# Kernel tuning notes

Measured on AMD Instinct MI355X. Metric: run time of the kernel, lower is better.

## Reference

```python
import jax, jax.numpy as jnp
import numpy as np

N_NODES = 100_000
N_EDGES = 1_600_000
HIDDEN = 64
EPS = 1e-5  # eqx.nn.RMSNorm default eps


def setup_inputs() -> dict:
    key = jax.random.key(0)
    k1, k2, k3 = jax.random.split(key, 3)
    x = jax.random.normal(k1, (N_NODES, HIDDEN), dtype=jnp.float32)
    # edges[0] = target node i, edges[1] = source node j  (a[i, j] = 1 => edge j -> i)
    edges = jax.random.randint(k2, (2, N_EDGES), 0, N_NODES, dtype=jnp.int32)
    W = jax.random.normal(k3, (HIDDEN, HIDDEN), dtype=jnp.float32) * (1.0 / np.sqrt(HIDDEN))
    b = jnp.zeros((HIDDEN,), dtype=jnp.float32)
    norm_weight = jnp.ones((HIDDEN,), dtype=jnp.float32)
    norm_bias = jnp.zeros((HIDDEN,), dtype=jnp.float32)
    return {"x": x, "edges": edges, "W": W, "b": b,
            "norm_weight": norm_weight, "norm_bias": norm_bias}


def reference(x, edges, W, b, norm_weight, norm_bias):
    n_nodes = x.shape[0]
    # vmap(Linear) + relu:  m = relu(x @ W.T + b)
    m = jax.nn.relu(jnp.einsum('nd,kd->nk', x, W) + b)
    # a @ m : sum-aggregate messages from source j into target i
    dst, src = edges[0], edges[1]
    agg = jax.ops.segment_sum(m[src], dst, num_segments=n_nodes)
    # residual + RMSNorm (per-node)
    h = x + agg
    inv_rms = jax.lax.rsqrt(jnp.mean(h * h, axis=-1, keepdims=True) + EPS)
    return norm_weight * (h * inv_rms) + norm_bias
```

## Files before the change

### kernel.cpp

```cpp
#include <hip/hip_runtime.h>
#include <hip/hip_bf16.h>

#define N_NODES 100000
#define N_EDGES 1600000
#define HID 64

#define NG 196
#define GROUPS 511
#define GSTRIDE 512
#define NREP 2
#define RCAP 2048
#define EPT 8
#define BIN_BLOCKS 391
#define LCAP 48

using bf16 = __hip_bfloat16;
typedef __attribute__((ext_vector_type(8))) short short8;
typedef __attribute__((ext_vector_type(4))) float float4v;

__device__ __forceinline__ float bfbits2f(unsigned short u) {
    union { unsigned int i; float f; } v;
    v.i = ((unsigned int)u) << 16;
    return v.f;
}
__device__ __forceinline__ unsigned short f2bfbits(float f) {
    union { float f; unsigned int i; } v;
    v.f = f;
    unsigned int r = v.i + 0x7fffu + ((v.i >> 16) & 1u);
    return (unsigned short)(r >> 16);
}

__device__ __forceinline__ void load_frag_split(const float* __restrict__ p,
                                                short8& hi, short8& lo) {
    #pragma unroll
    for (int j = 0; j < 8; ++j) {
        const float f = p[j];
        const unsigned short h = f2bfbits(f);
        hi[j] = (short)h;
        lo[j] = (short)f2bfbits(f - bfbits2f(h));
    }
}

__global__ __launch_bounds__(256) void k_linear_mfma(
    const float* __restrict__ x, const float* __restrict__ W,
    const float* __restrict__ b, bf16* __restrict__ m)
{
    const int t = threadIdx.x;
    const int wv = t >> 6, l = t & 63;
    const int c = l & 15, q = l >> 4;
    const int tile = blockIdx.x * 4 + wv;
    if (tile >= N_NODES / 16) return;
    const int nb = tile * 16;

    short8 Bhi[4][2], Blo[4][2];
    #pragma unroll
    for (int nt = 0; nt < 4; ++nt)
        #pragma unroll
        for (int ks = 0; ks < 2; ++ks)
            load_frag_split(W + (size_t)(nt * 16 + c) * HID + ks * 32 + q * 8,
                            Bhi[nt][ks], Blo[nt][ks]);

    short8 Ahi[2], Alo[2];
    #pragma unroll
    for (int ks = 0; ks < 2; ++ks)
        load_frag_split(x + (size_t)(nb + c) * HID + ks * 32 + q * 8, Ahi[ks], Alo[ks]);

    float4v acc[4];
    #pragma unroll
    for (int nt = 0; nt < 4; ++nt) {
        const float bias = b[nt * 16 + c];
        acc[nt] = (float4v){bias, bias, bias, bias};
        #pragma unroll
        for (int ks = 0; ks < 2; ++ks) {
            acc[nt] = __builtin_amdgcn_mfma_f32_16x16x32_bf16(Ahi[ks], Bhi[nt][ks], acc[nt], 0, 0, 0);
            acc[nt] = __builtin_amdgcn_mfma_f32_16x16x32_bf16(Ahi[ks], Blo[nt][ks], acc[nt], 0, 0, 0);
            acc[nt] = __builtin_amdgcn_mfma_f32_16x16x32_bf16(Alo[ks], Bhi[nt][ks], acc[nt], 0, 0, 0);
        }
    }

    unsigned short* mp = reinterpret_cast<unsigned short*>(m);
    #pragma unroll
    for (int nt = 0; nt < 4; ++nt)
        #pragma unroll
        for (int rg = 0; rg < 4; ++rg) {
            const float v = fmaxf(acc[nt][rg], 0.0f);
            mp[(size_t)(nb + q * 4 + rg) * HID + nt * 16 + c] = f2bfbits(v);
        }
}

__global__ __launch_bounds__(512) void k_bin3(
    const int* __restrict__ edges, int* __restrict__ gcur, int* __restrict__ binned)
{
    __shared__ int cnt[GSTRIDE];
    __shared__ int base[GSTRIDE];
    const int t = threadIdx.x;
    for (int i = t; i < GSTRIDE; i += 512) cnt[i] = 0;
    __syncthreads();

    const int e0 = blockIdx.x * (512 * EPT);
    int gk[EPT], pk[EPT], sl[EPT];
    #pragma unroll
    for (int k = 0; k < EPT; ++k) {
        const int e = e0 + k * 512 + t;
        if (e < N_EDGES) {
            const int dst = edges[e];
            const int src = edges[N_EDGES + e];
            const int g = (int)((unsigned)dst / NG);
            gk[k] = g;
            pk[k] = ((dst - g * NG) << 17) | src;
            sl[k] = atomicAdd(&cnt[g], 1);
        } else gk[k] = -1;
    }
    __syncthreads();
    const int r = blockIdx.x & (NREP - 1);
    for (int i = t; i < GROUPS; i += 512) {
        const int cc = cnt[i];
        base[i] = cc ? atomicAdd(&gcur[r * GSTRIDE + i], cc) : 0;
    }
    __syncthreads();
    #pragma unroll
    for (int k = 0; k < EPT; ++k) {
        if (gk[k] >= 0) {
            const int pos = base[gk[k]] + sl[k];
            if (pos < RCAP)
                binned[(size_t)(r * GSTRIDE + gk[k]) * RCAP + pos] = pk[k];
        }
    }
}

__global__ __launch_bounds__(1024, 8) void k_gather_norm5(
    const float* __restrict__ x, const bf16* __restrict__ m,
    const int* __restrict__ gcur, const int* __restrict__ binned,
    const float* __restrict__ nw, const float* __restrict__ nb,
    float* __restrict__ out)
{
    __shared__ int lcount[NG];
    __shared__ int lsrc[NG * LCAP];
    const int t = threadIdx.x;
    const int g = blockIdx.x;
    for (int i = t; i < NG; i += 1024) lcount[i] = 0;
    __syncthreads();

    #pragma unroll
    for (int rr = 0; rr < NREP; ++rr) {
        int c = gcur[rr * GSTRIDE + g];
        if (c > RCAP) c = RCAP;
        const int* reg = binned + (size_t)(rr * GSTRIDE + g) * RCAP;
        for (int i = t; i < c; i += 1024) {
            const int pr = reg[i];
            const int dl = pr >> 17;
            const int slot = atomicAdd(&lcount[dl], 1);
            if (slot < LCAP) lsrc[dl * LCAP + slot] = pr & 0x1FFFF;
        }
    }
    __syncthreads();

    const int wv = t >> 6, l = t & 63;
    const int c = l & 15;
    const int r = l >> 4;
    const ushort4* mu4 = reinterpret_cast<const ushort4*>(m);
    const float4 nw4 = reinterpret_cast<const float4*>(nw)[c];
    const float4 nb4 = reinterpret_cast<const float4*>(nb)[c];

    for (int dl = wv; dl < NG; dl += 16) {
        const int n = g * NG + dl;
        if (n >= N_NODES) break;
        int deg = lcount[dl]; if (deg > LCAP) deg = LCAP;
        const int* row = &lsrc[dl * LCAP];

        float4 a = make_float4(0.f, 0.f, 0.f, 0.f);
        int i = 0;
        for (; i + 16 <= deg; i += 16) {
            const int s0 = row[i + r];
            const int s1 = row[i + 4 + r];
            const int s2 = row[i + 8 + r];
            const int s3 = row[i + 12 + r];
            const ushort4 v0 = mu4[(size_t)s0 * 16 + c];
            const ushort4 v1 = mu4[(size_t)s1 * 16 + c];
            const ushort4 v2 = mu4[(size_t)s2 * 16 + c];
            const ushort4 v3 = mu4[(size_t)s3 * 16 + c];
            a.x += (bfbits2f(v0.x) + bfbits2f(v1.x)) + (bfbits2f(v2.x) + bfbits2f(v3.x));
            a.y += (bfbits2f(v0.y) + bfbits2f(v1.y)) + (bfbits2f(v2.y) + bfbits2f(v3.y));
            a.z += (bfbits2f(v0.z) + bfbits2f(v1.z)) + (bfbits2f(v2.z) + bfbits2f(v3.z));
            a.w += (bfbits2f(v0.w) + bfbits2f(v1.w)) + (bfbits2f(v2.w) + bfbits2f(v3.w));
        }
        for (; i < deg; i += 4) {
            const int e = i + r;
            if (e < deg) {
                const ushort4 v = mu4[(size_t)row[e] * 16 + c];
                a.x += bfbits2f(v.x);
                a.y += bfbits2f(v.y);
                a.z += bfbits2f(v.z);
                a.w += bfbits2f(v.w);
            }
        }
        a.x += __shfl_xor(a.x, 16, 64); a.x += __shfl_xor(a.x, 32, 64);
        a.y += __shfl_xor(a.y, 16, 64); a.y += __shfl_xor(a.y, 32, 64);
        a.z += __shfl_xor(a.z, 16, 64); a.z += __shfl_xor(a.z, 32, 64);
        a.w += __shfl_xor(a.w, 16, 64); a.w += __shfl_xor(a.w, 32, 64);

        const float4 x4 = reinterpret_cast<const float4*>(x)[(size_t)n * 16 + c];
        float4 h;
        h.x = x4.x + a.x; h.y = x4.y + a.y; h.z = x4.z + a.z; h.w = x4.w + a.w;
        float ss = h.x * h.x + h.y * h.y + h.z * h.z + h.w * h.w;
        ss += __shfl_xor(ss, 1, 64);
        ss += __shfl_xor(ss, 2, 64);
        ss += __shfl_xor(ss, 4, 64);
        ss += __shfl_xor(ss, 8, 64);
        const float inv = rsqrtf(ss * (1.0f / HID) + 1e-5f);
        if (r == 0) {
            float4 o;
            o.x = nw4.x * h.x * inv + nb4.x;
            o.y = nw4.y * h.y * inv + nb4.y;
            o.z = nw4.z * h.z * inv + nb4.z;
            o.w = nw4.w * h.w * inv + nb4.w;
            reinterpret_cast<float4*>(out)[(size_t)n * 16 + c] = o;
        }
    }
}

extern "C" void kernel_launch(void* const* d_in, const int* in_sizes, int n_in,
                              void* d_out, int out_size, void* d_ws, size_t ws_size,
                              hipStream_t stream) {
    const float* x     = (const float*)d_in[0];
    const int*   edges = (const int*)d_in[1];
    const float* W     = (const float*)d_in[2];
    const float* b     = (const float*)d_in[3];
    const float* nw    = (const float*)d_in[4];
    const float* nb    = (const float*)d_in[5];
    float* out = (float*)d_out;

    int*  gcur   = (int*)d_ws;
    int*  binned = (int*)((char*)d_ws + (1 << 16));
    bf16* m      = (bf16*)((char*)d_ws + (1 << 16) +
                           (size_t)NREP * GSTRIDE * RCAP * sizeof(int));

    hipMemsetAsync(gcur, 0, NREP * GSTRIDE * sizeof(int), stream);

    k_linear_mfma<<<(N_NODES / 16 + 3) / 4, 256, 0, stream>>>(x, W, b, m);
    k_bin3<<<BIN_BLOCKS, 512, 0, stream>>>(edges, gcur, binned);
    k_gather_norm5<<<GROUPS, 1024, 0, stream>>>(x, m, gcur, binned, nw, nb, out);
}
```

Before: 156.3 us.

## Fuse linear and edge binning into one launch, presplit W, batch gather loads

Replaces the memset with a small init kernel that zeroes counters and pre-splits W into bf16 hi/lo once. The linear and edge-binning kernels are merged into one heterogeneous launch of 256-thread blocks with EPT doubled, letting the two independent phases run concurrently. The linear pass drops the x low-part MFMA term, trading some accuracy for fewer MFMAs. The gather loop now issues eight clamped loads before accumulating, increasing memory-level parallelism.

```diff
diff --git a/kernel.cpp b/kernel.cpp
--- a/kernel.cpp
+++ b/kernel.cpp
@@ -10,8 +10,9 @@
 #define GSTRIDE 512
 #define NREP 2
 #define RCAP 2048
-#define EPT 8
+#define EPT 16
 #define BIN_BLOCKS 391
+#define LIN_BLOCKS 1563
 #define LCAP 48
 
 using bf16 = __hip_bfloat16;
@@ -30,105 +31,116 @@
     return (unsigned short)(r >> 16);
 }
 
-__device__ __forceinline__ void load_frag_split(const float* __restrict__ p,
-                                                short8& hi, short8& lo) {
-    #pragma unroll
-    for (int j = 0; j < 8; ++j) {
-        const float f = p[j];
+__global__ __launch_bounds__(256) void k_init(
+    const float* __restrict__ W, int* __restrict__ gcur,
+    unsigned short* __restrict__ Whi, unsigned short* __restrict__ Wlo)
+{
+    const int t = blockIdx.x * 256 + threadIdx.x;
+    for (int i = t; i < NREP * GSTRIDE; i += 512) gcur[i] = 0;
+    for (int i = t; i < HID * HID; i += 512) {
+        const float f = W[i];
         const unsigned short h = f2bfbits(f);
-        hi[j] = (short)h;
-        lo[j] = (short)f2bfbits(f - bfbits2f(h));
-    }
-}
-
-__global__ __launch_bounds__(256) void k_linear_mfma(
-    const float* __restrict__ x, const float* __restrict__ W,
-    const float* __restrict__ b, bf16* __restrict__ m)
+        Whi[i] = h;
+        Wlo[i] = f2bfbits(f - bfbits2f(h));
+    }
+}
+
+__global__ __launch_bounds__(256, 4) void k_prep2(
+    const float* __restrict__ x, const unsigned short* __restrict__ Whi,
+    const unsigned short* __restrict__ Wlo, const float* __restrict__ b,
+    bf16* __restrict__ m,
+    const int* __restrict__ edges, int* __restrict__ gcur,
+    int* __restrict__ binned)
 {
     const int t = threadIdx.x;
-    const int wv = t >> 6, l = t & 63;
-    const int c = l & 15, q = l >> 4;
-    const int tile = blockIdx.x * 4 + wv;
-    if (tile >= N_NODES / 16) return;
-    const int nb = tile * 16;
-
-    short8 Bhi[4][2], Blo[4][2];
-    #pragma unroll
-    for (int nt = 0; nt < 4; ++nt)
+
+    if (blockIdx.x < LIN_BLOCKS) {
+        const int wv = t >> 6, l = t & 63;
+        const int c = l & 15, q = l >> 4;
+        const int tile = blockIdx.x * 4 + wv;
+        if (tile >= N_NODES / 16) return;
+        const int nb = tile * 16;
+
+        const short8* whi8 = reinterpret_cast<const short8*>(Whi);
+        const short8* wlo8 = reinterpret_cast<const short8*>(Wlo);
+        short8 Bhi[4][2], Blo[4][2];
+        #pragma unroll
+        for (int nt = 0; nt < 4; ++nt)
+            #pragma unroll
+            for (int ks = 0; ks < 2; ++ks) {
+                const int fi = (nt * 16 + c) * 8 + ks * 4 + q;
+                Bhi[nt][ks] = whi8[fi];
+                Blo[nt][ks] = wlo8[fi];
+            }
+
+        const float* xrow = x + (size_t)(nb + c) * HID;
+        short8 Ahi[2];
         #pragma unroll
         for (int ks = 0; ks < 2; ++ks)
-            load_frag_split(W + (size_t)(nt * 16 + c) * HID + ks * 32 + q * 8,
-                            Bhi[nt][ks], Blo[nt][ks]);
-
-    short8 Ahi[2], Alo[2];
-    #pragma unroll
-    for (int ks = 0; ks < 2; ++ks)
-        load_frag_split(x + (size_t)(nb + c) * HID + ks * 32 + q * 8, Ahi[ks], Alo[ks]);
-
-    float4v acc[4];
-    #pragma unroll
-    for (int nt = 0; nt < 4; ++nt) {
-        const float bias = b[nt * 16 + c];
-        acc[nt] = (float4v){bias, bias, bias, bias};
-        #pragma unroll
-        for (int ks = 0; ks < 2; ++ks) {
-            acc[nt] = __builtin_amdgcn_mfma_f32_16x16x32_bf16(Ahi[ks], Bhi[nt][ks], acc[nt], 0, 0, 0);
-            acc[nt] = __builtin_amdgcn_mfma_f32_16x16x32_bf16(Ahi[ks], Blo[nt][ks], acc[nt], 0, 0, 0);
-            acc[nt] = __builtin_amdgcn_mfma_f32_16x16x32_bf16(Alo[ks], Bhi[nt][ks], acc[nt], 0, 0, 0);
-        }
-    }
-
-    unsigned short* mp = reinterpret_cast<unsigned short*>(m);
-    #pragma unroll
-    for (int nt = 0; nt < 4; ++nt)
-        #pragma unroll
-        for (int rg = 0; rg < 4; ++rg) {
-            const float v = fmaxf(acc[nt][rg], 0.0f);
-            mp[(size_t)(nb + q * 4 + rg) * HID + nt * 16 + c] = f2bfbits(v);
-        }
-}
-
-__global__ __launch_bounds__(512) void k_bin3(
-    const int* __restrict__ edges, int* __restrict__ gcur, int* __restrict__ binned)
-{
-    __shared__ int cnt[GSTRIDE];
-    __shared__ int base[GSTRIDE];
-    const int t = threadIdx.x;
-    for (int i = t; i < GSTRIDE; i += 512) cnt[i] = 0;
-    __syncthreads();
-
-    const int e0 = blockIdx.x * (512 * EPT);
-    int gk[EPT], pk[EPT], sl[EPT];
-    #pragma unroll
-    for (int k = 0; k < EPT; ++k) {
-        const int e = e0 + k * 512 + t;
-        if (e < N_EDGES) {
-            const int dst = edges[e];
-            const int src = edges[N_EDGES + e];
-            const int g = (int)((unsigned)dst / NG);
-            gk[k] = g;
-            pk[k] = ((dst - g * NG) << 17) | src;
-            sl[k] = atomicAdd(&cnt[g], 1);
-        } else gk[k] = -1;
-    }
-    __syncthreads();
-    const int r = blockIdx.x & (NREP - 1);
-    for (int i = t; i < GROUPS; i += 512) {
-        const int cc = cnt[i];
-        base[i] = cc ? atomicAdd(&gcur[r * GSTRIDE + i], cc) : 0;
-    }
-    __syncthreads();
-    #pragma unroll
-    for (int k = 0; k < EPT; ++k) {
-        if (gk[k] >= 0) {
-            const int pos = base[gk[k]] + sl[k];
-            if (pos < RCAP)
-                binned[(size_t)(r * GSTRIDE + gk[k]) * RCAP + pos] = pk[k];
-        }
-    }
-}
-
-__global__ __launch_bounds__(1024, 8) void k_gather_norm5(
+            #pragma unroll
+            for (int j = 0; j < 8; ++j)
+                Ahi[ks][j] = (short)f2bfbits(xrow[ks * 32 + q * 8 + j]);
+
+        float4v acc[4];
+        #pragma unroll
+        for (int nt = 0; nt < 4; ++nt) {
+            const float bias = b[nt * 16 + c];
+            acc[nt] = (float4v){bias, bias, bias, bias};
+            #pragma unroll
+            for (int ks = 0; ks < 2; ++ks) {
+                acc[nt] = __builtin_amdgcn_mfma_f32_16x16x32_bf16(Ahi[ks], Bhi[nt][ks], acc[nt], 0, 0, 0);
+                acc[nt] = __builtin_amdgcn_mfma_f32_16x16x32_bf16(Ahi[ks], Blo[nt][ks], acc[nt], 0, 0, 0);
+            }
+        }
+
+        unsigned short* mp = reinterpret_cast<unsigned short*>(m);
+        #pragma unroll
+        for (int nt = 0; nt < 4; ++nt)
+            #pragma unroll
+            for (int rg = 0; rg < 4; ++rg) {
+                const float v = fmaxf(acc[nt][rg], 0.0f);
+                mp[(size_t)(nb + q * 4 + rg) * HID + nt * 16 + c] = f2bfbits(v);
+            }
+    } else {
+        __shared__ int cnt[GSTRIDE];
+        __shared__ int base[GSTRIDE];
+        const int bb = blockIdx.x - LIN_BLOCKS;
+        for (int i = t; i < GSTRIDE; i += 256) cnt[i] = 0;
+        __syncthreads();
+
+        const int e0 = bb * (256 * EPT);
+        int gk[EPT], pk[EPT], sl[EPT];
+        #pragma unroll
+        for (int k = 0; k < EPT; ++k) {
+            const int e = e0 + k * 256 + t;
+            if (e < N_EDGES) {
+                const int dst = edges[e];
+                const int src = edges[N_EDGES + e];
+                const int g = (int)((unsigned)dst / NG);
+                gk[k] = g;
+                pk[k] = ((dst - g * NG) << 17) | src;
+                sl[k] = atomicAdd(&cnt[g], 1);
+            } else gk[k] = -1;
+        }
+        __syncthreads();
+        const int r = bb & (NREP - 1);
+        for (int i = t; i < GROUPS; i += 256) {
+            const int cc = cnt[i];
+            base[i] = cc ? atomicAdd(&gcur[r * GSTRIDE + i], cc) : 0;
+        }
+        __syncthreads();
+        #pragma unroll
+        for (int k = 0; k < EPT; ++k) {
+            if (gk[k] >= 0) {
+                const int pos = base[gk[k]] + sl[k];
+                if ((unsigned)pos < RCAP)
+                    binned[(size_t)(r * GSTRIDE + gk[k]) * RCAP + pos] = pk[k];
+            }
+        }
+    }
+}
+
+__global__ __launch_bounds__(1024, 8) void k_gather_norm6(
     const float* __restrict__ x, const bf16* __restrict__ m,
     const int* __restrict__ gcur, const int* __restrict__ binned,
     const float* __restrict__ nw, const float* __restrict__ nb,
@@ -169,29 +181,23 @@
         const int* row = &lsrc[dl * LCAP];
 
         float4 a = make_float4(0.f, 0.f, 0.f, 0.f);
-        int i = 0;
-        for (; i + 16 <= deg; i += 16) {
-            const int s0 = row[i + r];
-            const int s1 = row[i + 4 + r];
-            const int s2 = row[i + 8 + r];
-            const int s3 = row[i + 12 + r];
-            const ushort4 v0 = mu4[(size_t)s0 * 16 + c];
-            const ushort4 v1 = mu4[(size_t)s1 * 16 + c];
-            const ushort4 v2 = mu4[(size_t)s2 * 16 + c];
-            const ushort4 v3 = mu4[(size_t)s3 * 16 + c];
-            a.x += (bfbits2f(v0.x) + bfbits2f(v1.x)) + (bfbits2f(v2.x) + bfbits2f(v3.x));
-            a.y += (bfbits2f(v0.y) + bfbits2f(v1.y)) + (bfbits2f(v2.y) + bfbits2f(v3.y));
-            a.z += (bfbits2f(v0.z) + bfbits2f(v1.z)) + (bfbits2f(v2.z) + bfbits2f(v3.z));
-            a.w += (bfbits2f(v0.w) + bfbits2f(v1.w)) + (bfbits2f(v2.w) + bfbits2f(v3.w));
-        }
-        for (; i < deg; i += 4) {
-            const int e = i + r;
-            if (e < deg) {
-                const ushort4 v = mu4[(size_t)row[e] * 16 + c];
-                a.x += bfbits2f(v.x);
-                a.y += bfbits2f(v.y);
-                a.z += bfbits2f(v.z);
-                a.w += bfbits2f(v.w);
+        for (int i0 = 0; i0 < deg; i0 += 32) {
+            ushort4 vb[8];
+            #pragma unroll
+            for (int j = 0; j < 8; ++j) {
+                const int e = i0 + j * 4 + r;
+                const int ec = (e < deg) ? e : (deg - 1);
+                vb[j] = mu4[(size_t)row[ec] * 16 + c];
+            }
+            #pragma unroll
+            for (int j = 0; j < 8; ++j) {
+                const int e = i0 + j * 4 + r;
+                if (e < deg) {
+                    a.x += bfbits2f(vb[j].x);
+                    a.y += bfbits2f(vb[j].y);
+                    a.z += bfbits2f(vb[j].z);
+                    a.w += bfbits2f(vb[j].w);
+                }
             }
         }
         a.x += __shfl_xor(a.x, 16, 64); a.x += __shfl_xor(a.x, 32, 64);
@@ -230,14 +236,14 @@
     const float* nb    = (const float*)d_in[5];
     float* out = (float*)d_out;
 
-    int*  gcur   = (int*)d_ws;
+    int* gcur = (int*)d_ws;
+    unsigned short* Whi = (unsigned short*)((char*)d_ws + (1 << 14));
+    unsigned short* Wlo = Whi + HID * HID;
     int*  binned = (int*)((char*)d_ws + (1 << 16));
     bf16* m      = (bf16*)((char*)d_ws + (1 << 16) +
                            (size_t)NREP * GSTRIDE * RCAP * sizeof(int));
 
-    hipMemsetAsync(gcur, 0, NREP * GSTRIDE * sizeof(int), stream);
-
-    k_linear_mfma<<<(N_NODES / 16 + 3) / 4, 256, 0, stream>>>(x, W, b, m);
-    k_bin3<<<BIN_BLOCKS, 512, 0, stream>>>(edges, gcur, binned);
-    k_gather_norm5<<<GROUPS, 1024, 0, stream>>>(x, m, gcur, binned, nw, nb, out);
-}
+    k_init<<<2, 256, 0, stream>>>(W, gcur, Whi, Wlo);
+    k_prep2<<<LIN_BLOCKS + BIN_BLOCKS, 256, 0, stream>>>(x, Whi, Wlo, b, m, edges, gcur, binned);
+    k_gather_norm6<<<GROUPS, 1024, 0, stream>>>(x, m, gcur, binned, nw, nb, out);
+}
```

Measured after the change: 156.0 us. No clear change (-0.2%).
